# Optimization experiments

Hardware: AMD Instinct MI355X
Metric: run time of the kernel (lower is better)

The kernel has to match this reference:

```python
import jax, jax.numpy as jnp
import numpy as np

DELTA = 5.0          # weight on positive BCE term
R = 0.01             # hard-negative fraction
M, N = 4096, 16384   # batch rows, memory-bank size
NUM_HARD = int(R * (N - 1))  # int(r * neg_count); each row has exactly 1 positive


def setup_inputs() -> dict:
    key = jax.random.key(0)
    k1, k2 = jax.random.split(key)
    inputs = jax.random.normal(k1, (M, N), dtype=jnp.float32)
    targets = jax.random.randint(k2, (M,), 0, N)
    return {"inputs": inputs, "targets": targets}


def reference(inputs, targets):
    m, n = inputs.shape
    rows = jnp.arange(m)
    # positive logit per row (one-hot scatter => exactly one positive)
    pos = inputs[rows, targets]                          # [m]
    # BCE with logits, target=1: softplus(-x); mean over the single positive
    l_pos = jax.nn.softplus(-pos)                        # [m]
    # exclude positive from negatives by sinking it to -inf, then hard top-k
    neg_inf = jnp.finfo(inputs.dtype).min
    masked = inputs.at[rows, targets].set(neg_inf)       # [m, n]
    hard_neg, _ = jax.lax.top_k(masked, NUM_HARD)        # [m, NUM_HARD]
    # BCE with logits, target=0: softplus(x); mean over hard negatives
    l_neg = jnp.mean(jax.nn.softplus(hard_neg), axis=1)  # [m]
    return jnp.mean(DELTA * l_pos + l_neg)
```

## Files before the change

kernel.cpp:

```cpp
#include <hip/hip_runtime.h>
#include <stdint.h>

#define M_ROWS 4096
#define N_COLS 16384
#define K_HARD 163
#define DELTA_W 5.0f
#define CAP    1024
#define NB1    4096
#define NB2    1024
#define BLOCK  256

__device__ __forceinline__ uint32_t f2key(float x) {
    uint32_t u = __float_as_uint(x);
    return u ^ (((int32_t)u >> 31) | 0x80000000u);
}
__device__ __forceinline__ float key2f(uint32_t k) {
    uint32_t u = (k & 0x80000000u) ? (k & 0x7fffffffu) : ~k;
    return __uint_as_float(u);
}
__device__ __forceinline__ float softplus_f(float x) {
    return fmaxf(x, 0.0f) + log1pf(__expf(-fabsf(x)));
}

#define KEY_MIN 0xC0000000u

__device__ void pivot_scan(const uint32_t* hist, int nb, int K,
                           int* part, int* pivot, int* krem) {
    const int t = threadIdx.x;
    const int bpt = nb / BLOCK;
    const int base = t * bpt;
    int mypart = 0;
    for (int i = 0; i < bpt; ++i) mypart += (int)hist[base + i];
    part[t] = mypart;
    __syncthreads();
    for (int off = 1; off < BLOCK; off <<= 1) {
        int v = part[t];
        if (t + off < BLOCK) v += part[t + off];
        __syncthreads();
        part[t] = v;
        __syncthreads();
    }
    const int above = part[t] - mypart;
    if (above < K && above + mypart >= K) {
        int running = above;
        for (int b = base + bpt - 1; b >= base; --b) {
            int c = (int)hist[b];
            if (running < K && running + c >= K) { *pivot = b; *krem = K - running; }
            running += c;
        }
    }
    __syncthreads();
}

__global__ __launch_bounds__(BLOCK) void mmcl_kernel(
        const float* __restrict__ inputs,
        const int* __restrict__ targets,
        float* __restrict__ out) {
    __shared__ uint32_t s_hist[NB1];
    __shared__ uint32_t s_cand[CAP];
    __shared__ int s_part[BLOCK];
    __shared__ int s_ncand;
    __shared__ int s_found;
    __shared__ int s_pivot;
    __shared__ int s_krem;
    __shared__ float s_pos;
    __shared__ float s_wsum[BLOCK / 64];

    const int row = blockIdx.x;
    const int t = threadIdx.x;
    const int lane = t & 63;
    const float* rowp = inputs + (size_t)row * N_COLS;
    const int target = targets[row];

    for (int i = t; i < NB1; i += BLOCK) s_hist[i] = 0;
    if (t == 0) { s_ncand = 0; s_found = -1; s_pos = rowp[target]; }
    __syncthreads();

    const float4* rp4 = (const float4*)rowp;
#pragma unroll 4
    for (int it = 0; it < N_COLS / (BLOCK * 4); ++it) {
        const float4 v = rp4[it * BLOCK + t];
        const uint32_t k0 = f2key(v.x), k1 = f2key(v.y),
                       k2 = f2key(v.z), k3 = f2key(v.w);
        if (k0 >= KEY_MIN) { int i = atomicAdd(&s_ncand, 1); if (i < CAP) s_cand[i] = k0; }
        if (k1 >= KEY_MIN) { int i = atomicAdd(&s_ncand, 1); if (i < CAP) s_cand[i] = k1; }
        if (k2 >= KEY_MIN) { int i = atomicAdd(&s_ncand, 1); if (i < CAP) s_cand[i] = k2; }
        if (k3 >= KEY_MIN) { int i = atomicAdd(&s_ncand, 1); if (i < CAP) s_cand[i] = k3; }
    }
    __syncthreads();

    const int ncand_raw = s_ncand;
    const uint32_t tkey = f2key(s_pos);
    const bool no_ovf = (ncand_raw <= CAP);
    if (no_ovf && tkey >= KEY_MIN) {
        for (int i = t; i < ncand_raw; i += BLOCK)
            if (s_cand[i] == tkey) { atomicCAS(&s_found, -1, i); break; }
    }
    __syncthreads();
    if (t == 0 && s_found >= 0) {
        s_cand[s_found] = s_cand[ncand_raw - 1];
        s_ncand = ncand_raw - 1;
    }
    __syncthreads();
    const int ncand = s_ncand;
    const bool fast = no_ovf && (ncand >= K_HARD);

    float local = 0.0f;
    uint32_t T;
    int tie;

    if (fast) {
        for (int i = t; i < ncand; i += BLOCK)
            atomicAdd(&s_hist[s_cand[i] >> 20], 1u);
        __syncthreads();
        pivot_scan(s_hist, NB1, K_HARD, s_part, &s_pivot, &s_krem);
        const int p1 = s_pivot, k1r = s_krem;

        for (int i = t; i < NB2; i += BLOCK) s_hist[i] = 0;
        __syncthreads();
        for (int i = t; i < ncand; i += BLOCK) {
            const uint32_t k = s_cand[i];
            if ((int)(k >> 20) == p1) atomicAdd(&s_hist[(k >> 10) & 1023u], 1u);
        }
        __syncthreads();
        pivot_scan(s_hist, NB2, k1r, s_part, &s_pivot, &s_krem);
        const int p2 = s_pivot, k2r = s_krem;
        const uint32_t pref2 = ((uint32_t)p1 << 10) | (uint32_t)p2;

        for (int i = t; i < NB2; i += BLOCK) s_hist[i] = 0;
        __syncthreads();
        for (int i = t; i < ncand; i += BLOCK) {
            const uint32_t k = s_cand[i];
            if ((k >> 10) == pref2) atomicAdd(&s_hist[k & 1023u], 1u);
        }
        __syncthreads();
        pivot_scan(s_hist, NB2, k2r, s_part, &s_pivot, &s_krem);
        T = (pref2 << 10) | (uint32_t)s_pivot;
        tie = s_krem;

        for (int i = t; i < ncand; i += BLOCK) {
            const uint32_t k = s_cand[i];
            if (k > T) local += softplus_f(key2f(k));
        }
    } else {
        for (int i = t; i < NB1; i += BLOCK) s_hist[i] = 0;
        __syncthreads();
        for (int j = t; j < N_COLS; j += BLOCK) {
            if (j == target) continue;
            atomicAdd(&s_hist[f2key(rowp[j]) >> 20], 1u);
        }
        __syncthreads();
        pivot_scan(s_hist, NB1, K_HARD, s_part, &s_pivot, &s_krem);
        const int p1 = s_pivot, k1r = s_krem;

        for (int i = t; i < NB2; i += BLOCK) s_hist[i] = 0;
        __syncthreads();
        for (int j = t; j < N_COLS; j += BLOCK) {
            if (j == target) continue;
            const uint32_t k = f2key(rowp[j]);
            if ((int)(k >> 20) == p1) atomicAdd(&s_hist[(k >> 10) & 1023u], 1u);
        }
        __syncthreads();
        pivot_scan(s_hist, NB2, k1r, s_part, &s_pivot, &s_krem);
        const int p2 = s_pivot, k2r = s_krem;
        const uint32_t pref2 = ((uint32_t)p1 << 10) | (uint32_t)p2;

        for (int i = t; i < NB2; i += BLOCK) s_hist[i] = 0;
        __syncthreads();
        for (int j = t; j < N_COLS; j += BLOCK) {
            if (j == target) continue;
            const uint32_t k = f2key(rowp[j]);
            if ((k >> 10) == pref2) atomicAdd(&s_hist[k & 1023u], 1u);
        }
        __syncthreads();
        pivot_scan(s_hist, NB2, k2r, s_part, &s_pivot, &s_krem);
        T = (pref2 << 10) | (uint32_t)s_pivot;
        tie = s_krem;

        for (int j = t; j < N_COLS; j += BLOCK) {
            if (j == target) continue;
            const uint32_t k = f2key(rowp[j]);
            if (k > T) local += softplus_f(key2f(k));
        }
    }

    for (int off = 32; off > 0; off >>= 1) local += __shfl_down(local, off);
    if (lane == 0) s_wsum[t >> 6] = local;
    __syncthreads();
    if (t == 0) {
        float tot = 0.0f;
        for (int w = 0; w < BLOCK / 64; ++w) tot += s_wsum[w];
        tot += (float)tie * softplus_f(key2f(T));
        const float l_neg = tot / (float)K_HARD;
        const float l_pos = softplus_f(-s_pos);
        const float rowval = (DELTA_W * l_pos + l_neg) * (1.0f / (float)M_ROWS);
        atomicAdd(out, rowval);
    }
}

__global__ void mmcl_zero_out(float* out) { out[0] = 0.0f; }

extern "C" void kernel_launch(void* const* d_in, const int* in_sizes, int n_in,
                              void* d_out, int out_size, void* d_ws, size_t ws_size,
                              hipStream_t stream) {
    const float* inputs = (const float*)d_in[0];
    const int* targets = (const int*)d_in[1];
    float* out = (float*)d_out;
    mmcl_zero_out<<<1, 1, 0, stream>>>(out);
    mmcl_kernel<<<M_ROWS, BLOCK, 0, stream>>>(inputs, targets, out);
}
```

Before: 400.3 us.

## Use per-wave ballot compaction for candidates and shrink histogram LDS

Candidate gathering now uses a wave ballot with mbcnt prefix counts into per-wave buffers, replacing contended shared-memory atomics on a single counter, and then compacts the buffers into one array. Candidate keys always fall above a known bound, so the first-level histogram is biased and shrunk from 4096 to 1024 bins, which cuts the zeroing and scan work and lowers LDS use per block. The slow fallback path becomes a 4-level radix select (10/10/10/2 bits). Costs are an extra compaction pass with a second candidate buffer, and a per-wave capacity of 256 that can overflow sooner than the old shared cap of 1024.

```diff
diff --git a/kernel.cpp b/kernel.cpp
--- a/kernel.cpp
+++ b/kernel.cpp
@@ -5,14 +5,18 @@
 #define N_COLS 16384
 #define K_HARD 163
 #define DELTA_W 5.0f
-#define CAP    1024
-#define NB1    4096
-#define NB2    1024
+#define CAPW   256
+#define NWAVE  4
+#define CAP    (CAPW * NWAVE)
+#define NB     1024
 #define BLOCK  256
+
+#define KEY_MIN  0xC0000000u
+#define BIN_BIAS 3072
 
 __device__ __forceinline__ uint32_t f2key(float x) {
     uint32_t u = __float_as_uint(x);
-    return u ^ (((int32_t)u >> 31) | 0x80000000u);
+    return u ^ (uint32_t)(((int32_t)u >> 31) | 0x80000000u);
 }
 __device__ __forceinline__ float key2f(uint32_t k) {
     uint32_t u = (k & 0x80000000u) ? (k & 0x7fffffffu) : ~k;
@@ -22,12 +26,10 @@
     return fmaxf(x, 0.0f) + log1pf(__expf(-fabsf(x)));
 }
 
-#define KEY_MIN 0xC0000000u
-
-__device__ void pivot_scan(const uint32_t* hist, int nb, int K,
+__device__ void pivot_scan(const uint32_t* hist, int K,
                            int* part, int* pivot, int* krem) {
     const int t = threadIdx.x;
-    const int bpt = nb / BLOCK;
+    const int bpt = NB / BLOCK;
     const int base = t * bpt;
     int mypart = 0;
     for (int i = 0; i < bpt; ++i) mypart += (int)hist[base + i];
@@ -56,53 +58,76 @@
         const float* __restrict__ inputs,
         const int* __restrict__ targets,
         float* __restrict__ out) {
-    __shared__ uint32_t s_hist[NB1];
+    __shared__ uint32_t s_hist[NB];
     __shared__ uint32_t s_cand[CAP];
+    __shared__ uint32_t s_cand2[CAP];
     __shared__ int s_part[BLOCK];
-    __shared__ int s_ncand;
+    __shared__ int s_cnt[NWAVE];
     __shared__ int s_found;
     __shared__ int s_pivot;
     __shared__ int s_krem;
-    __shared__ float s_pos;
-    __shared__ float s_wsum[BLOCK / 64];
+    __shared__ float s_wsum[NWAVE];
 
     const int row = blockIdx.x;
     const int t = threadIdx.x;
     const int lane = t & 63;
+    const int wid = t >> 6;
     const float* rowp = inputs + (size_t)row * N_COLS;
     const int target = targets[row];
 
-    for (int i = t; i < NB1; i += BLOCK) s_hist[i] = 0;
-    if (t == 0) { s_ncand = 0; s_found = -1; s_pos = rowp[target]; }
-    __syncthreads();
-
+    for (int i = t; i < NB; i += BLOCK) s_hist[i] = 0;
+    if (t == 0) s_found = -1;
+
+    uint32_t* wcand = s_cand + wid * CAPW;
+    int wcount = 0;
     const float4* rp4 = (const float4*)rowp;
 #pragma unroll 4
     for (int it = 0; it < N_COLS / (BLOCK * 4); ++it) {
         const float4 v = rp4[it * BLOCK + t];
-        const uint32_t k0 = f2key(v.x), k1 = f2key(v.y),
-                       k2 = f2key(v.z), k3 = f2key(v.w);
-        if (k0 >= KEY_MIN) { int i = atomicAdd(&s_ncand, 1); if (i < CAP) s_cand[i] = k0; }
-        if (k1 >= KEY_MIN) { int i = atomicAdd(&s_ncand, 1); if (i < CAP) s_cand[i] = k1; }
-        if (k2 >= KEY_MIN) { int i = atomicAdd(&s_ncand, 1); if (i < CAP) s_cand[i] = k2; }
-        if (k3 >= KEY_MIN) { int i = atomicAdd(&s_ncand, 1); if (i < CAP) s_cand[i] = k3; }
-    }
-    __syncthreads();
-
-    const int ncand_raw = s_ncand;
-    const uint32_t tkey = f2key(s_pos);
-    const bool no_ovf = (ncand_raw <= CAP);
+        const float vals[4] = {v.x, v.y, v.z, v.w};
+#pragma unroll
+        for (int c = 0; c < 4; ++c) {
+            const uint32_t k = f2key(vals[c]);
+            const bool pred = (k >= KEY_MIN);
+            const unsigned long long mask = __ballot(pred);
+            if (pred) {
+                const int below = __builtin_amdgcn_mbcnt_hi(
+                    (uint32_t)(mask >> 32),
+                    __builtin_amdgcn_mbcnt_lo((uint32_t)mask, 0));
+                const int off = wcount + below;
+                if (off < CAPW) wcand[off] = k;
+            }
+            wcount += (int)__popcll(mask);
+        }
+    }
+    if (lane == 0) s_cnt[wid] = wcount;
+    __syncthreads();
+
+    const int c0 = s_cnt[0], c1 = s_cnt[1], c2 = s_cnt[2], c3 = s_cnt[3];
+    const int total = c0 + c1 + c2 + c3;
+    const bool no_ovf = (c0 <= CAPW) & (c1 <= CAPW) & (c2 <= CAPW) & (c3 <= CAPW);
+    const int wbase = (wid > 0 ? c0 : 0) + (wid > 1 ? c1 : 0) + (wid > 2 ? c2 : 0);
+
+    const float pos = rowp[target];
+    const uint32_t tkey = f2key(pos);
+
+    if (no_ovf) {
+        const int mycnt = s_cnt[wid];
+        for (int i = lane; i < mycnt; i += 64) s_cand2[wbase + i] = wcand[i];
+    }
+    __syncthreads();
+
     if (no_ovf && tkey >= KEY_MIN) {
-        for (int i = t; i < ncand_raw; i += BLOCK)
-            if (s_cand[i] == tkey) { atomicCAS(&s_found, -1, i); break; }
-    }
-    __syncthreads();
-    if (t == 0 && s_found >= 0) {
-        s_cand[s_found] = s_cand[ncand_raw - 1];
-        s_ncand = ncand_raw - 1;
-    }
-    __syncthreads();
-    const int ncand = s_ncand;
+        for (int i = t; i < total; i += BLOCK)
+            if (s_cand2[i] == tkey) { atomicCAS(&s_found, -1, i); break; }
+    }
+    __syncthreads();
+    int ncand = total;
+    if (s_found >= 0) {
+        if (t == 0) s_cand2[s_found] = s_cand2[total - 1];
+        ncand = total - 1;
+    }
+    __syncthreads();
     const bool fast = no_ovf && (ncand >= K_HARD);
 
     float local = 0.0f;
@@ -111,70 +136,92 @@
 
     if (fast) {
         for (int i = t; i < ncand; i += BLOCK)
-            atomicAdd(&s_hist[s_cand[i] >> 20], 1u);
-        __syncthreads();
-        pivot_scan(s_hist, NB1, K_HARD, s_part, &s_pivot, &s_krem);
-        const int p1 = s_pivot, k1r = s_krem;
-
-        for (int i = t; i < NB2; i += BLOCK) s_hist[i] = 0;
+            atomicAdd(&s_hist[(s_cand2[i] >> 20) - BIN_BIAS], 1u);
+        __syncthreads();
+        pivot_scan(s_hist, K_HARD, s_part, &s_pivot, &s_krem);
+        const int p1b = s_pivot + BIN_BIAS, k1r = s_krem;
+
+        for (int i = t; i < NB; i += BLOCK) s_hist[i] = 0;
         __syncthreads();
         for (int i = t; i < ncand; i += BLOCK) {
-            const uint32_t k = s_cand[i];
-            if ((int)(k >> 20) == p1) atomicAdd(&s_hist[(k >> 10) & 1023u], 1u);
-        }
-        __syncthreads();
-        pivot_scan(s_hist, NB2, k1r, s_part, &s_pivot, &s_krem);
+            const uint32_t k = s_cand2[i];
+            if ((int)(k >> 20) == p1b) atomicAdd(&s_hist[(k >> 10) & 1023u], 1u);
+        }
+        __syncthreads();
+        pivot_scan(s_hist, k1r, s_part, &s_pivot, &s_krem);
         const int p2 = s_pivot, k2r = s_krem;
-        const uint32_t pref2 = ((uint32_t)p1 << 10) | (uint32_t)p2;
-
-        for (int i = t; i < NB2; i += BLOCK) s_hist[i] = 0;
+        const uint32_t pref2 = ((uint32_t)p1b << 10) | (uint32_t)p2;
+
+        for (int i = t; i < NB; i += BLOCK) s_hist[i] = 0;
         __syncthreads();
         for (int i = t; i < ncand; i += BLOCK) {
-            const uint32_t k = s_cand[i];
+            const uint32_t k = s_cand2[i];
             if ((k >> 10) == pref2) atomicAdd(&s_hist[k & 1023u], 1u);
         }
         __syncthreads();
-        pivot_scan(s_hist, NB2, k2r, s_part, &s_pivot, &s_krem);
+        pivot_scan(s_hist, k2r, s_part, &s_pivot, &s_krem);
         T = (pref2 << 10) | (uint32_t)s_pivot;
         tie = s_krem;
 
         for (int i = t; i < ncand; i += BLOCK) {
-            const uint32_t k = s_cand[i];
+            const uint32_t k = s_cand2[i];
             if (k > T) local += softplus_f(key2f(k));
         }
     } else {
-        for (int i = t; i < NB1; i += BLOCK) s_hist[i] = 0;
-        __syncthreads();
-        for (int j = t; j < N_COLS; j += BLOCK) {
-            if (j == target) continue;
-            atomicAdd(&s_hist[f2key(rowp[j]) >> 20], 1u);
-        }
-        __syncthreads();
-        pivot_scan(s_hist, NB1, K_HARD, s_part, &s_pivot, &s_krem);
+        for (int i = t; i < NB; i += BLOCK) s_hist[i] = 0;
+        __syncthreads();
+        for (int j = t; j < N_COLS; j += BLOCK) {
+            if (j == target) continue;
+            atomicAdd(&s_hist[f2key(rowp[j]) >> 22], 1u);
+        }
+        __syncthreads();
+        pivot_scan(s_hist, K_HARD, s_part, &s_pivot, &s_krem);
         const int p1 = s_pivot, k1r = s_krem;
 
-        for (int i = t; i < NB2; i += BLOCK) s_hist[i] = 0;
-        __syncthreads();
-        for (int j = t; j < N_COLS; j += BLOCK) {
-            if (j == target) continue;
-            const uint32_t k = f2key(rowp[j]);
-            if ((int)(k >> 20) == p1) atomicAdd(&s_hist[(k >> 10) & 1023u], 1u);
-        }
-        __syncthreads();
-        pivot_scan(s_hist, NB2, k1r, s_part, &s_pivot, &s_krem);
-        const int p2 = s_pivot, k2r = s_krem;
-        const uint32_t pref2 = ((uint32_t)p1 << 10) | (uint32_t)p2;
-
-        for (int i = t; i < NB2; i += BLOCK) s_hist[i] = 0;
-        __syncthreads();
-        for (int j = t; j < N_COLS; j += BLOCK) {
-            if (j == target) continue;
-            const uint32_t k = f2key(rowp[j]);
-            if ((k >> 10) == pref2) atomicAdd(&s_hist[k & 1023u], 1u);
-        }
-        __syncthreads();
-        pivot_scan(s_hist, NB2, k2r, s_part, &s_pivot, &s_krem);
-        T = (pref2 << 10) | (uint32_t)s_pivot;
+        for (int i = t; i < NB; i += BLOCK) s_hist[i] = 0;
+        __syncthreads();
+        for (int j = t; j < N_COLS; j += BLOCK) {
+            if (j == target) continue;
+            const uint32_t k = f2key(rowp[j]);
+            if ((int)(k >> 22) == p1) atomicAdd(&s_hist[(k >> 12) & 1023u], 1u);
+        }
+        __syncthreads();
+        pivot_scan(s_hist, k1r, s_part, &s_pivot, &s_krem);
+        const uint32_t pref2 = ((uint32_t)p1 << 10) | (uint32_t)s_pivot;
+        const int k2r = s_krem;
+
+        for (int i = t; i < NB; i += BLOCK) s_hist[i] = 0;
+        __syncthreads();
+        for (int j = t; j < N_COLS; j += BLOCK) {
+            if (j == target) continue;
+            const uint32_t k = f2key(rowp[j]);
+            if ((k >> 12) == pref2) atomicAdd(&s_hist[(k >> 2) & 1023u], 1u);
+        }
+        __syncthreads();
+        pivot_scan(s_hist, k2r, s_part, &s_pivot, &s_krem);
+        const uint32_t pref3 = (pref2 << 10) | (uint32_t)s_pivot;
+        const int k3r = s_krem;
+
+        for (int i = t; i < NB; i += BLOCK) s_hist[i] = 0;
+        __syncthreads();
+        for (int j = t; j < N_COLS; j += BLOCK) {
+            if (j == target) continue;
+            const uint32_t k = f2key(rowp[j]);
+            if ((k >> 2) == pref3) atomicAdd(&s_hist[k & 3u], 1u);
+        }
+        __syncthreads();
+        if (t == 0) {
+            int running = 0;
+            for (int b = 3; b >= 0; --b) {
+                const int c = (int)s_hist[b];
+                if (running < k3r && running + c >= k3r) {
+                    s_pivot = b; s_krem = k3r - running;
+                }
+                running += c;
+            }
+        }
+        __syncthreads();
+        T = (pref3 << 2) | (uint32_t)s_pivot;
         tie = s_krem;
 
         for (int j = t; j < N_COLS; j += BLOCK) {
@@ -185,14 +232,14 @@
     }
 
     for (int off = 32; off > 0; off >>= 1) local += __shfl_down(local, off);
-    if (lane == 0) s_wsum[t >> 6] = local;
+    if (lane == 0) s_wsum[wid] = local;
     __syncthreads();
     if (t == 0) {
         float tot = 0.0f;
-        for (int w = 0; w < BLOCK / 64; ++w) tot += s_wsum[w];
+        for (int w = 0; w < NWAVE; ++w) tot += s_wsum[w];
         tot += (float)tie * softplus_f(key2f(T));
         const float l_neg = tot / (float)K_HARD;
-        const float l_pos = softplus_f(-s_pos);
+        const float l_pos = softplus_f(-pos);
         const float rowval = (DELTA_W * l_pos + l_neg) * (1.0f / (float)M_ROWS);
         atomicAdd(out, rowval);
     }
```

Measured after the change: 382.5 us. -4.4%, faster.
